# Kernel tuning notes

Hardware: AMD Instinct MI355X
Metric: run time of the kernel (lower is better)

The kernel has to match this reference:

```python
import jax, jax.numpy as jnp
import numpy as np
from jax import lax

B, T, I = 256, 720, 16   # batch, seq_len, input_dim
H = 128                  # hidden_dim
PRED_LEN = 96


def lstm_cell(x, h, c, W_ih, W_hh, b):
    # PyTorch gate order: i, f, g, o ; b = b_ih + b_hh (combined)
    gates = x @ W_ih.T + h @ W_hh.T + b
    i, f, g, o = jnp.split(gates, 4, axis=-1)
    c = jax.nn.sigmoid(f) * c + jax.nn.sigmoid(i) * jnp.tanh(g)
    h = jax.nn.sigmoid(o) * jnp.tanh(c)
    return h, c


def setup_inputs() -> dict:
    key = jax.random.key(0)
    ks = jax.random.split(key, 16)
    k = 1.0 / np.sqrt(H)
    u = lambda kk, shape: jax.random.uniform(kk, shape, jnp.float32, -k, k)
    inp = {
        "x": jax.random.normal(ks[0], (B, T, I), jnp.float32),
        # encoder (bidirectional, 1 layer): forward + backward directions
        "e_Wih_f": u(ks[1], (4 * H, I)), "e_Whh_f": u(ks[2], (4 * H, H)), "e_b_f": u(ks[3], (4 * H,)),
        "e_Wih_b": u(ks[4], (4 * H, I)), "e_Whh_b": u(ks[5], (4 * H, H)), "e_b_b": u(ks[6], (4 * H,)),
        # decoder (bidirectional, 1 layer)
        "d_Wih_f": u(ks[7], (4 * H, I)), "d_Whh_f": u(ks[8], (4 * H, H)), "d_b_f": u(ks[9], (4 * H,)),
        "d_Wih_b": u(ks[10], (4 * H, I)), "d_Whh_b": u(ks[11], (4 * H, H)), "d_b_b": u(ks[12], (4 * H,)),
        # final linear: (2H -> I)
        "W_lin": u(ks[13], (I, 2 * H)), "b_lin": u(ks[14], (I,)),
    }
    return inp


def reference(x, e_Wih_f, e_Whh_f, e_b_f, e_Wih_b, e_Whh_b, e_b_b,
              d_Wih_f, d_Whh_f, d_b_f, d_Wih_b, d_Whh_b, d_b_b,
              W_lin, b_lin):
    xt = jnp.transpose(x, (1, 0, 2))  # [T, B, I] time-major
    h0 = jnp.zeros((B, H), x.dtype)
    c0 = jnp.zeros((B, H), x.dtype)

    # ---- encoder: bidirectional LSTM; only final (h, c) per direction is used ----
    def enc_f(carry, xt_t):
        h, c = lstm_cell(xt_t, carry[0], carry[1], e_Wih_f, e_Whh_f, e_b_f)
        return (h, c), None

    def enc_b(carry, xt_t):
        h, c = lstm_cell(xt_t, carry[0], carry[1], e_Wih_b, e_Whh_b, e_b_b)
        return (h, c), None

    (hf, cf), _ = lax.scan(enc_f, (h0, c0), xt)
    (hb, cb), _ = lax.scan(enc_b, (h0, c0), xt[::-1])

    def dec_step(carry, _):
        inp, hf, cf, hb, cb = carry
        hf, cf = lstm_cell(inp, hf, cf, d_Wih_f, d_Whh_f, d_b_f)
        hb, cb = lstm_cell(inp, hb, cb, d_Wih_b, d_Whh_b, d_b_b)
        # seq_len==1 so out_f = forward hidden, out_b = backward hidden
        out = jnp.concatenate([hf, hb], axis=-1) @ W_lin.T + b_lin  # [B, I]
        return (out, hf, cf, hb, cb), out

    init = (x[:, -1, :], hf, cf, hb, cb)
    _, outs = lax.scan(dec_step, init, None, length=PRED_LEN)  # [P, B, I]
    return jnp.transpose(outs, (1, 0, 2))  # [B, pred_len, I]
```

## Files before the change

kernel.cpp:

```cpp
#include <hip/hip_runtime.h>
#include <math.h>

#define TB    720
#define NI    16
#define NH    128
#define NG    512
#define PRED  96
#define CHUNK 90

typedef _Float16 h2    __attribute__((ext_vector_type(2)));
typedef _Float16 f16x4 __attribute__((ext_vector_type(4)));
typedef _Float16 f16x8 __attribute__((ext_vector_type(8)));
typedef float    f32x4 __attribute__((ext_vector_type(4)));

#define LOG2E  1.4426950408889634f
#define LOG2E2 2.8853900817779268f

__device__ __forceinline__ float rcpf_(float v) {
#if __has_builtin(__builtin_amdgcn_rcpf)
    return __builtin_amdgcn_rcpf(v);
#else
    return 1.0f / v;
#endif
}
__device__ __forceinline__ float ex2(float v) {
#if __has_builtin(__builtin_amdgcn_exp2f)
    return __builtin_amdgcn_exp2f(v);
#else
    return exp2f(v);
#endif
}
__device__ __forceinline__ float sigf(float v)   { return rcpf_(1.0f + __expf(-v)); }
__device__ __forceinline__ float tanhf_(float v) { return 1.0f - 2.0f * rcpf_(1.0f + __expf(2.0f * v)); }

__device__ __forceinline__ unsigned int packf16(float a, float b) {
    h2 p; p.x = (_Float16)a; p.y = (_Float16)b;
    return __builtin_bit_cast(unsigned int, p);
}
__device__ __forceinline__ float2 unpackf16(unsigned int u) {
    h2 p = __builtin_bit_cast(h2, u);
    return make_float2((float)p.x, (float)p.y);
}
__device__ __forceinline__ float fdot2f(unsigned int a, unsigned int b, float c) {
#if __has_builtin(__builtin_amdgcn_fdot2)
    return __builtin_amdgcn_fdot2(__builtin_bit_cast(h2, a), __builtin_bit_cast(h2, b), c, false);
#else
    h2 x = __builtin_bit_cast(h2, a), y = __builtin_bit_cast(h2, b);
    return c + (float)x.x * (float)y.x + (float)x.y * (float)y.y;
#endif
}

__device__ __forceinline__ f16x8 mk8s(const float* p, float s) {
    f16x8 v;
    v[0] = (_Float16)(p[0]  * s); v[1] = (_Float16)(p[1]  * s);
    v[2] = (_Float16)(p[2]  * s); v[3] = (_Float16)(p[3]  * s);
    v[4] = (_Float16)(p[16] * s); v[5] = (_Float16)(p[17] * s);
    v[6] = (_Float16)(p[18] * s); v[7] = (_Float16)(p[19] * s);
    return v;
}
__device__ __forceinline__ f32x4 MFMA(f16x8 a, f16x8 b, f32x4 c) {
    return __builtin_amdgcn_mfma_f32_16x16x32_f16(a, b, c, 0, 0, 0);
}

template <int CTRL, int RMASK>
__device__ __forceinline__ float dppadd(float v) {
    int s = __builtin_bit_cast(int, v);
    int d = __builtin_amdgcn_update_dpp(0, s, CTRL, RMASK, 0xf, true);
    return v + __builtin_bit_cast(float, d);
}

__global__ __launch_bounds__(1024, 4)
void enc_kernel(const float* __restrict__ x,
                const float* __restrict__ Wih_f, const float* __restrict__ Whh_f, const float* __restrict__ b_f,
                const float* __restrict__ Wih_b, const float* __restrict__ Whh_b, const float* __restrict__ b_b,
                float* __restrict__ st)
{
    __shared__ _Float16 hbuf0[16 * NH];
    __shared__ _Float16 hbuf1[16 * NH];
    __shared__ unsigned int xsh[CHUNK * 128];

    const int blk = blockIdx.x;
    const int dir = blk & 1;
    const int b0  = (blk >> 1) << 4;
    const int t   = threadIdx.x;
    const int wv  = t >> 6;
    const int l   = t & 63;
    const int lr  = l & 15;
    const int lk  = l >> 4;

    const float* Wih = dir ? Wih_b : Wih_f;
    const float* Whh = dir ? Whh_b : Whh_f;
    const float* bv  = dir ? b_b   : b_f;

    const int mt0 = 2 * wv, mt1 = 2 * wv + 1;
    const int R0 = mt0 * 16 + lr, R1 = mt1 * 16 + lr;
    const int or0 = (R0 & 3) * 128 + (R0 >> 2);
    const int or1 = (R1 & 3) * 128 + (R1 >> 2);
    const float s0 = ((or0 >> 7) == 2) ? LOG2E2 : LOG2E;
    const float s1 = ((or1 >> 7) == 2) ? LOG2E2 : LOG2E;
    const float* p0 = Whh + (size_t)or0 * NH + lk * 4;
    const float* p1 = Whh + (size_t)or1 * NH + lk * 4;
    f16x8 w0_0 = mk8s(p0, s0), w0_1 = mk8s(p0 + 32, s0), w0_2 = mk8s(p0 + 64, s0), w0_3 = mk8s(p0 + 96, s0);
    f16x8 w1_0 = mk8s(p1, s1), w1_1 = mk8s(p1 + 32, s1), w1_2 = mk8s(p1 + 64, s1), w1_3 = mk8s(p1 + 96, s1);

    f16x8 ax0, ax1;
#define MKAXR(DST, OR, SC) { \
    const float* xr_ = Wih + (size_t)(OR) * NI + lk * 4; \
    DST[0] = (_Float16)(xr_[0] * (SC)); DST[1] = (_Float16)(xr_[1] * (SC)); \
    DST[2] = (_Float16)(xr_[2] * (SC)); DST[3] = (_Float16)(xr_[3] * (SC)); \
    DST[4] = (_Float16)(bv[(OR)] * (SC)); \
    DST[5] = (_Float16)0.f; DST[6] = (_Float16)0.f; DST[7] = (_Float16)0.f; }
    MKAXR(ax0, or0, s0) MKAXR(ax1, or1, s1)
#undef MKAXR

    const int d0 = mt0 * 4 + lk, d1 = mt1 * 4 + lk;

    ((unsigned int*)hbuf0)[t] = 0u;
    float cs0 = 0.f, cs1 = 0.f;

    const int hro0 = 0 * 1024 + lk * 256 + lr * 16;
    const int hro1 = 1 * 1024 + lk * 256 + lr * 16;
    const int hro2 = 2 * 1024 + lk * 256 + lr * 16;
    const int hro3 = 3 * 1024 + lk * 256 + lr * 16;
#define CWB(D) ((((D) >> 5) * 1024) + ((((D) & 15) >> 2) * 256) + lr * 16 + (((((D) & 31) >> 4) * 4 + ((D) & 3)) * 2))
    const int cwb0 = CWB(d0), cwb1 = CWB(d1);
#undef CWB
    const int xoff = lk * 128 + lr * 8;
    const unsigned int oneku = (lk == 0) ? 0x00003c00u : 0u;
    const f32x4 CZ = {0.f, 0.f, 0.f, 0.f};
    __syncthreads();

#define CELL(J, HW) { \
    float ei_ = ex2(-C##J[0]), ef_ = ex2(-C##J[1]); \
    float eg_ = ex2(C##J[2]),  eo_ = ex2(-C##J[3]); \
    float di_ = 1.f + ei_, df_ = 1.f + ef_, dg_ = 1.f + eg_, dq_ = 1.f + eo_; \
    float r1_ = rcpf_(di_ * df_), r2_ = rcpf_(dq_ * dg_); \
    float si_ = r1_ * df_, sf_ = r1_ * di_, so_ = r2_ * dg_; \
    float tg_ = __builtin_fmaf(-2.f * r2_, dq_, 1.f); \
    cs##J = sf_ * cs##J + si_ * tg_; \
    float ec_ = ex2(cs##J * LOG2E2); \
    float th_ = __builtin_fmaf(-2.f, rcpf_(1.f + ec_), 1.f); \
    float hv_ = so_ * th_; \
    *(_Float16*)((char*)(HW) + cwb##J) = (_Float16)hv_; }

#define STEP(HR, HW, SI) { \
    const char* hrb_ = (const char*)(HR); \
    f16x8 bx; \
    { uint2 xq_ = *(const uint2*)((const char*)xsh + (SI) * 512 + xoff); \
      ((unsigned int*)&bx)[0] = xq_.x; ((unsigned int*)&bx)[1] = xq_.y; \
      ((unsigned int*)&bx)[2] = oneku; ((unsigned int*)&bx)[3] = 0u; } \
    f32x4 C0 = MFMA(ax0, bx, CZ); \
    f32x4 C1 = MFMA(ax1, bx, CZ); \
    f16x8 bh_; \
    bh_ = *(const f16x8*)(hrb_ + hro0); \
    C0 = MFMA(w0_0, bh_, C0); C1 = MFMA(w1_0, bh_, C1); \
    bh_ = *(const f16x8*)(hrb_ + hro1); \
    C0 = MFMA(w0_1, bh_, C0); C1 = MFMA(w1_1, bh_, C1); \
    bh_ = *(const f16x8*)(hrb_ + hro2); \
    C0 = MFMA(w0_2, bh_, C0); C1 = MFMA(w1_2, bh_, C1); \
    bh_ = *(const f16x8*)(hrb_ + hro3); \
    C0 = MFMA(w0_3, bh_, C0); C1 = MFMA(w1_3, bh_, C1); \
    CELL(0, HW) CELL(1, HW) \
    __syncthreads(); }

    for (int c = 0; c < 8; ++c) {
        {
            const int c0 = c * CHUNK;
            for (int i = t; i < 16 * CHUNK * 8; i += 1024) {
                const int br  = i / (CHUNK * 8);
                const int rem = i - br * (CHUNK * 8);
                const int ti  = rem >> 3;
                const int dw  = rem & 7;
                const int s_  = c0 + ti;
                const int tt  = dir ? (TB - 1 - s_) : s_;
                float2 v = *(const float2*)(x + ((size_t)(b0 + br) * TB + tt) * NI + dw * 2);
                xsh[ti * 128 + (dw >> 1) * 32 + br * 2 + (dw & 1)] = packf16(v.x, v.y);
            }
        }
        __syncthreads();
        for (int si2 = 0; si2 < CHUNK / 2; ++si2) {
            STEP(hbuf0, hbuf1, si2 * 2)
            STEP(hbuf1, hbuf0, si2 * 2 + 1)
        }
    }
#undef STEP
#undef CELL

    {
        const size_t base = ((size_t)(b0 + lr) * 2 + dir) * 2 * NH;
#define FIN(J) { \
        float hv_ = (float)*(const _Float16*)((const char*)hbuf0 + cwb##J); \
        st[base + d##J] = hv_; st[base + NH + d##J] = cs##J; }
        FIN(0) FIN(1)
#undef FIN
    }
}

#define R8(F)  F(0)F(1)F(2)F(3)F(4)F(5)F(6)F(7)
#define R36_(F) F(8)F(9)F(10)F(11)F(12)F(13)F(14)F(15)F(16)F(17)F(18)F(19)F(20)F(21)F(22)F(23)F(24)F(25)F(26)F(27)F(28)F(29)F(30)F(31)F(32)F(33)F(34)F(35)
#define R36(F) R8(F) R36_(F)
#define R64(F) R36(F) F(36)F(37)F(38)F(39)F(40)F(41)F(42)F(43)F(44)F(45)F(46)F(47)F(48)F(49)F(50)F(51)F(52)F(53)F(54)F(55)F(56)F(57)F(58)F(59)F(60)F(61)F(62)F(63)

#define QD(Q,i0,i1,i2,i3) { a0 = fdot2f((Q).x, w##i0, a0); a1 = fdot2f((Q).y, w##i1, a1); \
                            a2 = fdot2f((Q).z, w##i2, a2); a3 = fdot2f((Q).w, w##i3, a3); }
#define QDU(Q,i0,i1,i2,i3) { a0 = fdot2f((Q).x, u##i0, a0); a1 = fdot2f((Q).y, u##i1, a1); \
                             a2 = fdot2f((Q).z, u##i2, a2); a3 = fdot2f((Q).w, u##i3, a3); }

__global__ __launch_bounds__(1024, 1)
void dec_kernel(const float* __restrict__ x,
                const float* __restrict__ Wih_f, const float* __restrict__ Whh_f, const float* __restrict__ b_f,
                const float* __restrict__ Wih_b, const float* __restrict__ Whh_b, const float* __restrict__ b_b,
                const float* __restrict__ Wlin, const float* __restrict__ blin,
                const float* __restrict__ st, float* __restrict__ out)
{
    __shared__ unsigned int hFh[NH / 2], hBh[NH / 2];
    __shared__ unsigned int inpH[NI / 2];
    __shared__ float g[1024];
    __shared__ float obuf[PRED * 16];

    const int b    = blockIdx.x;
    const int t    = threadIdx.x;
    const int cell = t >> 9;
    const int r    = t & 511;
    const int w    = t >> 6;
    const int ln   = t & 63;

    const float* Wih = cell ? Wih_b : Wih_f;
    const float* Whh = cell ? Whh_b : Whh_f;
    const float* bv  = cell ? b_b   : b_f;

#define DW(K) unsigned int w##K;
    R64(DW)
#undef DW
#define DU(K) unsigned int u##K;
    R8(DU)
#undef DU
    {
        const float* xr = Wih + r * NI;
        const float* hr = Whh + r * NH;
#define LU(K) u##K = packf16(xr[2*(K)], xr[2*(K)+1]);
        R8(LU)
#undef LU
#define LH(K) w##K = packf16(hr[2*(K)], hr[2*(K)+1]);
        R64(LH)
#undef LH
    }
    const float bias = bv[r];

    const float wl0 = Wlin[w * 256 + ln * 4 + 0];
    const float wl1 = Wlin[w * 256 + ln * 4 + 1];
    const float wl2 = Wlin[w * 256 + ln * 4 + 2];
    const float wl3 = Wlin[w * 256 + ln * 4 + 3];
    const float blw = blin[w];

    float cc = 0.0f;
    if (t < 64) {
        const float* sh = st + ((b * 2 + 0) * 2 + 0) * NH;
        hFh[t] = packf16(sh[2 * t], sh[2 * t + 1]);
    } else if (t < 128) {
        const float* sh = st + ((b * 2 + 1) * 2 + 0) * NH;
        hBh[t - 64] = packf16(sh[2 * (t - 64)], sh[2 * (t - 64) + 1]);
    }
    if (t < NH) cc = st[((b * 2 + 0) * 2 + 1) * NH + t];
    else if (t >= 512 && t < 512 + NH) cc = st[((b * 2 + 1) * 2 + 1) * NH + (t - 512)];
    if (t < 8) {
        float2 v = ((const float2*)(x + (size_t)b * TB * NI + (TB - 1) * NI))[t];
        inpH[t] = packf16(v.x, v.y);
    }
    __syncthreads();

    for (int s = 0; s < PRED; ++s) {
        float a0 = bias, a1 = 0.f, a2 = 0.f, a3 = 0.f;
        uint4 q;
        {
            const uint4* xv = (const uint4*)inpH;
            q = xv[0]; QDU(q, 0, 1, 2, 3)
            q = xv[1]; QDU(q, 4, 5, 6, 7)
        }
        const uint4* hv = cell ? (const uint4*)hBh : (const uint4*)hFh;
        q = hv[0];  QD(q, 0, 1, 2, 3)
        q = hv[1];  QD(q, 4, 5, 6, 7)
        q = hv[2];  QD(q, 8, 9, 10, 11)
        q = hv[3];  QD(q, 12, 13, 14, 15)
        q = hv[4];  QD(q, 16, 17, 18, 19)
        q = hv[5];  QD(q, 20, 21, 22, 23)
        q = hv[6];  QD(q, 24, 25, 26, 27)
        q = hv[7];  QD(q, 28, 29, 30, 31)
        q = hv[8];  QD(q, 32, 33, 34, 35)
        q = hv[9];  QD(q, 36, 37, 38, 39)
        q = hv[10]; QD(q, 40, 41, 42, 43)
        q = hv[11]; QD(q, 44, 45, 46, 47)
        q = hv[12]; QD(q, 48, 49, 50, 51)
        q = hv[13]; QD(q, 52, 53, 54, 55)
        q = hv[14]; QD(q, 56, 57, 58, 59)
        q = hv[15]; QD(q, 60, 61, 62, 63)
        g[t] = (a0 + a1) + (a2 + a3);
        __syncthreads();

        if ((t < NH) || (t >= 512 && t < 512 + NH)) {
            float gi = g[t], gf = g[t + NH], gg = g[t + 2 * NH], go = g[t + 3 * NH];
            cc = sigf(gf) * cc + sigf(gi) * tanhf_(gg);
            float h = sigf(go) * tanhf_(cc);
            if (t < NH) ((_Float16*)hFh)[t] = (_Float16)h;
            else        ((_Float16*)hBh)[t - 512] = (_Float16)h;
        }
        __syncthreads();

        {
            const unsigned int* hsrc = (ln < 32) ? (hFh + 2 * ln) : (hBh + 2 * (ln - 32));
            uint2 hw = *(const uint2*)hsrc;
            float2 va = unpackf16(hw.x), vb = unpackf16(hw.y);
            float p = va.x * wl0 + va.y * wl1 + vb.x * wl2 + vb.y * wl3;
            p = dppadd<0x111, 0xf>(p);
            p = dppadd<0x112, 0xf>(p);
            p = dppadd<0x114, 0xf>(p);
            p = dppadd<0x118, 0xf>(p);
            p = dppadd<0x142, 0xa>(p);
            p = dppadd<0x143, 0xc>(p);
            if (ln == 63) {
                float o = p + blw;
                obuf[s * NI + w] = o;
                ((_Float16*)inpH)[w] = (_Float16)o;
            }
        }
        __syncthreads();
    }

    {
        float4* dst = (float4*)(out + (size_t)b * PRED * NI);
        const float4* src = (const float4*)obuf;
        for (int i = t; i < PRED * NI / 4; i += 1024) dst[i] = src[i];
    }
}

extern "C" void kernel_launch(void* const* d_in, const int* in_sizes, int n_in,
                              void* d_out, int out_size, void* d_ws, size_t ws_size,
                              hipStream_t stream)
{
    const float* x      = (const float*)d_in[0];
    const float* eWih_f = (const float*)d_in[1];
    const float* eWhh_f = (const float*)d_in[2];
    const float* eb_f   = (const float*)d_in[3];
    const float* eWih_b = (const float*)d_in[4];
    const float* eWhh_b = (const float*)d_in[5];
    const float* eb_b   = (const float*)d_in[6];
    const float* dWih_f = (const float*)d_in[7];
    const float* dWhh_f = (const float*)d_in[8];
    const float* db_f   = (const float*)d_in[9];
    const float* dWih_b = (const float*)d_in[10];
    const float* dWhh_b = (const float*)d_in[11];
    const float* db_b   = (const float*)d_in[12];
    const float* Wlin   = (const float*)d_in[13];
    const float* blin   = (const float*)d_in[14];

    float* st = (float*)d_ws;

    enc_kernel<<<32, 1024, 0, stream>>>(x, eWih_f, eWhh_f, eb_f, eWih_b, eWhh_b, eb_b, st);
    dec_kernel<<<256, 1024, 0, stream>>>(x, dWih_f, dWhh_f, db_f, dWih_b, dWhh_b, db_b,
                                         Wlin, blin, st, (float*)d_out);
}
```

Measured before the change: 717.1 us.

## Batch decoder over 16 samples per block using MFMA for gates and linear

Replaces the per-sample decoder, which did one block per batch element using packed fp16 dot products, with a batched decoder that handles 16 samples per block. Gate matmuls and the output linear projection run on MFMA instructions, reusing the encoder's layout and fused sigmoid/tanh cell math. This aims to cut per-step latency and sync count in the autoregressive loop. It adds a large shared output buffer and leaves only 16 blocks, so occupancy is low.

```diff
diff --git a/kernel.cpp b/kernel.cpp
--- a/kernel.cpp
+++ b/kernel.cpp
@@ -30,26 +30,14 @@
     return exp2f(v);
 #endif
 }
-__device__ __forceinline__ float sigf(float v)   { return rcpf_(1.0f + __expf(-v)); }
-__device__ __forceinline__ float tanhf_(float v) { return 1.0f - 2.0f * rcpf_(1.0f + __expf(2.0f * v)); }
 
 __device__ __forceinline__ unsigned int packf16(float a, float b) {
     h2 p; p.x = (_Float16)a; p.y = (_Float16)b;
     return __builtin_bit_cast(unsigned int, p);
 }
-__device__ __forceinline__ float2 unpackf16(unsigned int u) {
-    h2 p = __builtin_bit_cast(h2, u);
-    return make_float2((float)p.x, (float)p.y);
-}
-__device__ __forceinline__ float fdot2f(unsigned int a, unsigned int b, float c) {
-#if __has_builtin(__builtin_amdgcn_fdot2)
-    return __builtin_amdgcn_fdot2(__builtin_bit_cast(h2, a), __builtin_bit_cast(h2, b), c, false);
-#else
-    h2 x = __builtin_bit_cast(h2, a), y = __builtin_bit_cast(h2, b);
-    return c + (float)x.x * (float)y.x + (float)x.y * (float)y.y;
-#endif
-}
-
+__device__ __forceinline__ f32x4 MFMA(f16x8 a, f16x8 b, f32x4 c) {
+    return __builtin_amdgcn_mfma_f32_16x16x32_f16(a, b, c, 0, 0, 0);
+}
 __device__ __forceinline__ f16x8 mk8s(const float* p, float s) {
     f16x8 v;
     v[0] = (_Float16)(p[0]  * s); v[1] = (_Float16)(p[1]  * s);
@@ -58,16 +46,20 @@
     v[6] = (_Float16)(p[18] * s); v[7] = (_Float16)(p[19] * s);
     return v;
 }
-__device__ __forceinline__ f32x4 MFMA(f16x8 a, f16x8 b, f32x4 c) {
-    return __builtin_amdgcn_mfma_f32_16x16x32_f16(a, b, c, 0, 0, 0);
-}
-
-template <int CTRL, int RMASK>
-__device__ __forceinline__ float dppadd(float v) {
-    int s = __builtin_bit_cast(int, v);
-    int d = __builtin_amdgcn_update_dpp(0, s, CTRL, RMASK, 0xf, true);
-    return v + __builtin_bit_cast(float, d);
-}
+__device__ __forceinline__ int opaque(int v) { asm volatile("" : "+v"(v)); return v; }
+
+#define CELLBODY(CV, CS, HWPTR, CWBV) { \
+    float ei_ = ex2(-(CV)[0]), ef_ = ex2(-(CV)[1]); \
+    float eg_ = ex2((CV)[2]),  eo_ = ex2(-(CV)[3]); \
+    float di_ = 1.f + ei_, df_ = 1.f + ef_, dg_ = 1.f + eg_, dq_ = 1.f + eo_; \
+    float r1_ = rcpf_(di_ * df_), r2_ = rcpf_(dq_ * dg_); \
+    float si_ = r1_ * df_, sf_ = r1_ * di_, so_ = r2_ * dg_; \
+    float tg_ = __builtin_fmaf(-2.f * r2_, dq_, 1.f); \
+    (CS) = sf_ * (CS) + si_ * tg_; \
+    float ec_ = ex2((CS) * LOG2E2); \
+    float th_ = __builtin_fmaf(-2.f, rcpf_(1.f + ec_), 1.f); \
+    float hv_ = so_ * th_; \
+    *(_Float16*)((char*)(HWPTR) + (CWBV)) = (_Float16)hv_; }
 
 __global__ __launch_bounds__(1024, 4)
 void enc_kernel(const float* __restrict__ x,
@@ -129,19 +121,6 @@
     const unsigned int oneku = (lk == 0) ? 0x00003c00u : 0u;
     const f32x4 CZ = {0.f, 0.f, 0.f, 0.f};
     __syncthreads();
-
-#define CELL(J, HW) { \
-    float ei_ = ex2(-C##J[0]), ef_ = ex2(-C##J[1]); \
-    float eg_ = ex2(C##J[2]),  eo_ = ex2(-C##J[3]); \
-    float di_ = 1.f + ei_, df_ = 1.f + ef_, dg_ = 1.f + eg_, dq_ = 1.f + eo_; \
-    float r1_ = rcpf_(di_ * df_), r2_ = rcpf_(dq_ * dg_); \
-    float si_ = r1_ * df_, sf_ = r1_ * di_, so_ = r2_ * dg_; \
-    float tg_ = __builtin_fmaf(-2.f * r2_, dq_, 1.f); \
-    cs##J = sf_ * cs##J + si_ * tg_; \
-    float ec_ = ex2(cs##J * LOG2E2); \
-    float th_ = __builtin_fmaf(-2.f, rcpf_(1.f + ec_), 1.f); \
-    float hv_ = so_ * th_; \
-    *(_Float16*)((char*)(HW) + cwb##J) = (_Float16)hv_; }
 
 #define STEP(HR, HW, SI) { \
     const char* hrb_ = (const char*)(HR); \
@@ -160,7 +139,8 @@
     C0 = MFMA(w0_2, bh_, C0); C1 = MFMA(w1_2, bh_, C1); \
     bh_ = *(const f16x8*)(hrb_ + hro3); \
     C0 = MFMA(w0_3, bh_, C0); C1 = MFMA(w1_3, bh_, C1); \
-    CELL(0, HW) CELL(1, HW) \
+    CELLBODY(C0, cs0, HW, cwb0) \
+    CELLBODY(C1, cs1, HW, cwb1) \
     __syncthreads(); }
 
     for (int c = 0; c < 8; ++c) {
@@ -184,152 +164,170 @@
         }
     }
 #undef STEP
-#undef CELL
 
     {
         const size_t base = ((size_t)(b0 + lr) * 2 + dir) * 2 * NH;
-#define FIN(J) { \
-        float hv_ = (float)*(const _Float16*)((const char*)hbuf0 + cwb##J); \
-        st[base + d##J] = hv_; st[base + NH + d##J] = cs##J; }
-        FIN(0) FIN(1)
-#undef FIN
-    }
-}
-
-#define R8(F)  F(0)F(1)F(2)F(3)F(4)F(5)F(6)F(7)
-#define R36_(F) F(8)F(9)F(10)F(11)F(12)F(13)F(14)F(15)F(16)F(17)F(18)F(19)F(20)F(21)F(22)F(23)F(24)F(25)F(26)F(27)F(28)F(29)F(30)F(31)F(32)F(33)F(34)F(35)
-#define R36(F) R8(F) R36_(F)
-#define R64(F) R36(F) F(36)F(37)F(38)F(39)F(40)F(41)F(42)F(43)F(44)F(45)F(46)F(47)F(48)F(49)F(50)F(51)F(52)F(53)F(54)F(55)F(56)F(57)F(58)F(59)F(60)F(61)F(62)F(63)
-
-#define QD(Q,i0,i1,i2,i3) { a0 = fdot2f((Q).x, w##i0, a0); a1 = fdot2f((Q).y, w##i1, a1); \
-                            a2 = fdot2f((Q).z, w##i2, a2); a3 = fdot2f((Q).w, w##i3, a3); }
-#define QDU(Q,i0,i1,i2,i3) { a0 = fdot2f((Q).x, u##i0, a0); a1 = fdot2f((Q).y, u##i1, a1); \
-                             a2 = fdot2f((Q).z, u##i2, a2); a3 = fdot2f((Q).w, u##i3, a3); }
-
-__global__ __launch_bounds__(1024, 1)
+#define CWB(D) ((((D) >> 5) * 1024) + ((((D) & 15) >> 2) * 256) + lr * 16 + (((((D) & 31) >> 4) * 4 + ((D) & 3)) * 2))
+        st[base + d0]      = (float)*(const _Float16*)((const char*)hbuf0 + CWB(d0));
+        st[base + NH + d0] = cs0;
+        st[base + d1]      = (float)*(const _Float16*)((const char*)hbuf0 + CWB(d1));
+        st[base + NH + d1] = cs1;
+#undef CWB
+    }
+}
+
+__global__ __launch_bounds__(1024, 4)
 void dec_kernel(const float* __restrict__ x,
                 const float* __restrict__ Wih_f, const float* __restrict__ Whh_f, const float* __restrict__ b_f,
                 const float* __restrict__ Wih_b, const float* __restrict__ Whh_b, const float* __restrict__ b_b,
                 const float* __restrict__ Wlin, const float* __restrict__ blin,
                 const float* __restrict__ st, float* __restrict__ out)
 {
-    __shared__ unsigned int hFh[NH / 2], hBh[NH / 2];
-    __shared__ unsigned int inpH[NI / 2];
-    __shared__ float g[1024];
-    __shared__ float obuf[PRED * 16];
-
-    const int b    = blockIdx.x;
+    __shared__ _Float16 hF0[16 * NH], hF1[16 * NH];
+    __shared__ _Float16 hB0[16 * NH], hB1[16 * NH];
+    __shared__ unsigned int wlin_s[8 * 64 * 4];
+    __shared__ unsigned int inpH[16 * 8];
+    __shared__ float obuf[PRED * 16 * 16];
+
+    const int b0   = blockIdx.x << 4;
     const int t    = threadIdx.x;
-    const int cell = t >> 9;
-    const int r    = t & 511;
-    const int w    = t >> 6;
-    const int ln   = t & 63;
+    const int wv   = t >> 6;
+    const int cell = wv >> 3;
+    const int wvv  = wv & 7;
+    const int l    = t & 63;
+    const int lr   = l & 15;
+    const int lk   = l >> 4;
 
     const float* Wih = cell ? Wih_b : Wih_f;
     const float* Whh = cell ? Whh_b : Whh_f;
     const float* bv  = cell ? b_b   : b_f;
 
-#define DW(K) unsigned int w##K;
-    R64(DW)
-#undef DW
-#define DU(K) unsigned int u##K;
-    R8(DU)
-#undef DU
+    if (t < 512) {
+        const int f = t >> 6, ll = t & 63;
+        const int elr = ll & 15, elk = ll >> 4;
+        const float* wr = Wlin + elr * 256 + f * 32 + elk * 4;
+        uint4 q;
+        q.x = packf16(wr[0],  wr[1]);  q.y = packf16(wr[2],  wr[3]);
+        q.z = packf16(wr[16], wr[17]); q.w = packf16(wr[18], wr[19]);
+        *(uint4*)&wlin_s[(f * 64 + ll) * 4] = q;
+    }
+
+    const int mt0 = 4 * wvv, mt1 = 4 * wvv + 1, mt2 = 4 * wvv + 2, mt3 = 4 * wvv + 3;
+    const int R0 = mt0 * 16 + lr, R1 = mt1 * 16 + lr, R2 = mt2 * 16 + lr, R3 = mt3 * 16 + lr;
+    const int or0 = (R0 & 3) * 128 + (R0 >> 2);
+    const int or1 = (R1 & 3) * 128 + (R1 >> 2);
+    const int or2 = (R2 & 3) * 128 + (R2 >> 2);
+    const int or3 = (R3 & 3) * 128 + (R3 >> 2);
+    const float s0 = ((or0 >> 7) == 2) ? LOG2E2 : LOG2E;
+    const float s1 = ((or1 >> 7) == 2) ? LOG2E2 : LOG2E;
+    const float s2 = ((or2 >> 7) == 2) ? LOG2E2 : LOG2E;
+    const float s3 = ((or3 >> 7) == 2) ? LOG2E2 : LOG2E;
+    const float* p0 = Whh + (size_t)or0 * NH + lk * 4;
+    const float* p1 = Whh + (size_t)or1 * NH + lk * 4;
+    const float* p2 = Whh + (size_t)or2 * NH + lk * 4;
+    const float* p3 = Whh + (size_t)or3 * NH + lk * 4;
+    f16x8 w0_0 = mk8s(p0, s0), w0_1 = mk8s(p0 + 32, s0), w0_2 = mk8s(p0 + 64, s0), w0_3 = mk8s(p0 + 96, s0);
+    f16x8 w1_0 = mk8s(p1, s1), w1_1 = mk8s(p1 + 32, s1), w1_2 = mk8s(p1 + 64, s1), w1_3 = mk8s(p1 + 96, s1);
+    f16x8 w2_0 = mk8s(p2, s2), w2_1 = mk8s(p2 + 32, s2), w2_2 = mk8s(p2 + 64, s2), w2_3 = mk8s(p2 + 96, s2);
+    f16x8 w3_0 = mk8s(p3, s3), w3_1 = mk8s(p3 + 32, s3), w3_2 = mk8s(p3 + 64, s3), w3_3 = mk8s(p3 + 96, s3);
+
+    f16x8 ax0, ax1, ax2, ax3;
+#define MKAXR(DST, OR, SC) { \
+    const float* xr_ = Wih + (size_t)(OR) * NI + lk * 4; \
+    DST[0] = (_Float16)(xr_[0] * (SC)); DST[1] = (_Float16)(xr_[1] * (SC)); \
+    DST[2] = (_Float16)(xr_[2] * (SC)); DST[3] = (_Float16)(xr_[3] * (SC)); \
+    DST[4] = (_Float16)(bv[(OR)] * (SC)); \
+    DST[5] = (_Float16)0.f; DST[6] = (_Float16)0.f; DST[7] = (_Float16)0.f; }
+    MKAXR(ax0, or0, s0) MKAXR(ax1, or1, s1) MKAXR(ax2, or2, s2) MKAXR(ax3, or3, s3)
+#undef MKAXR
+
+    const int d0 = mt0 * 4 + lk, d1 = mt1 * 4 + lk, d2 = mt2 * 4 + lk, d3 = mt3 * 4 + lk;
+
+    const int hro0 = 0 * 1024 + lk * 256 + lr * 16;
+    const int hro1 = 1 * 1024 + lk * 256 + lr * 16;
+    const int hro2 = 2 * 1024 + lk * 256 + lr * 16;
+    const int hro3 = 3 * 1024 + lk * 256 + lr * 16;
+#define CWB(D) ((((D) >> 5) * 1024) + ((((D) & 15) >> 2) * 256) + lr * 16 + (((((D) & 31) >> 4) * 4 + ((D) & 3)) * 2))
+    const int cwb0 = CWB(d0), cwb1 = CWB(d1), cwb2 = CWB(d2), cwb3 = CWB(d3);
+    float cs0, cs1, cs2, cs3;
     {
-        const float* xr = Wih + r * NI;
-        const float* hr = Whh + r * NH;
-#define LU(K) u##K = packf16(xr[2*(K)], xr[2*(K)+1]);
-        R8(LU)
-#undef LU
-#define LH(K) w##K = packf16(hr[2*(K)], hr[2*(K)+1]);
-        R64(LH)
-#undef LH
-    }
-    const float bias = bv[r];
-
-    const float wl0 = Wlin[w * 256 + ln * 4 + 0];
-    const float wl1 = Wlin[w * 256 + ln * 4 + 1];
-    const float wl2 = Wlin[w * 256 + ln * 4 + 2];
-    const float wl3 = Wlin[w * 256 + ln * 4 + 3];
-    const float blw = blin[w];
-
-    float cc = 0.0f;
-    if (t < 64) {
-        const float* sh = st + ((b * 2 + 0) * 2 + 0) * NH;
-        hFh[t] = packf16(sh[2 * t], sh[2 * t + 1]);
-    } else if (t < 128) {
-        const float* sh = st + ((b * 2 + 1) * 2 + 0) * NH;
-        hBh[t - 64] = packf16(sh[2 * (t - 64)], sh[2 * (t - 64) + 1]);
-    }
-    if (t < NH) cc = st[((b * 2 + 0) * 2 + 1) * NH + t];
-    else if (t >= 512 && t < 512 + NH) cc = st[((b * 2 + 1) * 2 + 1) * NH + (t - 512)];
-    if (t < 8) {
-        float2 v = ((const float2*)(x + (size_t)b * TB * NI + (TB - 1) * NI))[t];
-        inpH[t] = packf16(v.x, v.y);
-    }
+        _Float16* hini = cell ? hB0 : hF0;
+        const size_t bs = ((size_t)(b0 + lr) * 2 + cell) * 2 * NH;
+        *(_Float16*)((char*)hini + cwb0) = (_Float16)st[bs + d0];  cs0 = st[bs + NH + d0];
+        *(_Float16*)((char*)hini + cwb1) = (_Float16)st[bs + d1];  cs1 = st[bs + NH + d1];
+        *(_Float16*)((char*)hini + cwb2) = (_Float16)st[bs + d2];  cs2 = st[bs + NH + d2];
+        *(_Float16*)((char*)hini + cwb3) = (_Float16)st[bs + d3];  cs3 = st[bs + NH + d3];
+    }
+#undef CWB
+    if (t < 128) {
+        const int ilr = t >> 3, idw = t & 7;
+        const float2 v = *(const float2*)(x + ((size_t)(b0 + ilr) * TB + (TB - 1)) * NI + idw * 2);
+        inpH[ilr * 8 + idw] = packf16(v.x, v.y);
+    }
+    const float bl0 = blin[4 * lk + 0], bl1 = blin[4 * lk + 1];
+    const float bl2 = blin[4 * lk + 2], bl3 = blin[4 * lk + 3];
+    const unsigned int oneku = (lk == 0) ? 0x00003c00u : 0u;
+    const f32x4 CZ = {0.f, 0.f, 0.f, 0.f};
     __syncthreads();
 
-    for (int s = 0; s < PRED; ++s) {
-        float a0 = bias, a1 = 0.f, a2 = 0.f, a3 = 0.f;
-        uint4 q;
-        {
-            const uint4* xv = (const uint4*)inpH;
-            q = xv[0]; QDU(q, 0, 1, 2, 3)
-            q = xv[1]; QDU(q, 4, 5, 6, 7)
-        }
-        const uint4* hv = cell ? (const uint4*)hBh : (const uint4*)hFh;
-        q = hv[0];  QD(q, 0, 1, 2, 3)
-        q = hv[1];  QD(q, 4, 5, 6, 7)
-        q = hv[2];  QD(q, 8, 9, 10, 11)
-        q = hv[3];  QD(q, 12, 13, 14, 15)
-        q = hv[4];  QD(q, 16, 17, 18, 19)
-        q = hv[5];  QD(q, 20, 21, 22, 23)
-        q = hv[6];  QD(q, 24, 25, 26, 27)
-        q = hv[7];  QD(q, 28, 29, 30, 31)
-        q = hv[8];  QD(q, 32, 33, 34, 35)
-        q = hv[9];  QD(q, 36, 37, 38, 39)
-        q = hv[10]; QD(q, 40, 41, 42, 43)
-        q = hv[11]; QD(q, 44, 45, 46, 47)
-        q = hv[12]; QD(q, 48, 49, 50, 51)
-        q = hv[13]; QD(q, 52, 53, 54, 55)
-        q = hv[14]; QD(q, 56, 57, 58, 59)
-        q = hv[15]; QD(q, 60, 61, 62, 63)
-        g[t] = (a0 + a1) + (a2 + a3);
-        __syncthreads();
-
-        if ((t < NH) || (t >= 512 && t < 512 + NH)) {
-            float gi = g[t], gf = g[t + NH], gg = g[t + 2 * NH], go = g[t + 3 * NH];
-            cc = sigf(gf) * cc + sigf(gi) * tanhf_(gg);
-            float h = sigf(go) * tanhf_(cc);
-            if (t < NH) ((_Float16*)hFh)[t] = (_Float16)h;
-            else        ((_Float16*)hBh)[t - 512] = (_Float16)h;
-        }
-        __syncthreads();
-
-        {
-            const unsigned int* hsrc = (ln < 32) ? (hFh + 2 * ln) : (hBh + 2 * (ln - 32));
-            uint2 hw = *(const uint2*)hsrc;
-            float2 va = unpackf16(hw.x), vb = unpackf16(hw.y);
-            float p = va.x * wl0 + va.y * wl1 + vb.x * wl2 + vb.y * wl3;
-            p = dppadd<0x111, 0xf>(p);
-            p = dppadd<0x112, 0xf>(p);
-            p = dppadd<0x114, 0xf>(p);
-            p = dppadd<0x118, 0xf>(p);
-            p = dppadd<0x142, 0xa>(p);
-            p = dppadd<0x143, 0xc>(p);
-            if (ln == 63) {
-                float o = p + blw;
-                obuf[s * NI + w] = o;
-                ((_Float16*)inpH)[w] = (_Float16)o;
-            }
-        }
-        __syncthreads();
-    }
-
-    {
-        float4* dst = (float4*)(out + (size_t)b * PRED * NI);
-        const float4* src = (const float4*)obuf;
-        for (int i = t; i < PRED * NI / 4; i += 1024) dst[i] = src[i];
+#define STEPD(HRF, HWF, HRB, HWB, S) { \
+    const char* hr_ = cell ? (const char*)(HRB) : (const char*)(HRF); \
+    char*       hw_ = cell ? (char*)(HWB)       : (char*)(HWF); \
+    f16x8 bx; \
+    { uint2 xq_ = *(const uint2*)((const char*)inpH + lr * 32 + lk * 8); \
+      ((unsigned int*)&bx)[0] = xq_.x; ((unsigned int*)&bx)[1] = xq_.y; \
+      ((unsigned int*)&bx)[2] = oneku; ((unsigned int*)&bx)[3] = 0u; } \
+    f32x4 C0 = MFMA(ax0, bx, CZ); f32x4 C1 = MFMA(ax1, bx, CZ); \
+    f32x4 C2 = MFMA(ax2, bx, CZ); f32x4 C3 = MFMA(ax3, bx, CZ); \
+    f16x8 bh_; \
+    bh_ = *(const f16x8*)(hr_ + hro0); \
+    C0 = MFMA(w0_0, bh_, C0); C1 = MFMA(w1_0, bh_, C1); \
+    C2 = MFMA(w2_0, bh_, C2); C3 = MFMA(w3_0, bh_, C3); \
+    bh_ = *(const f16x8*)(hr_ + hro1); \
+    C0 = MFMA(w0_1, bh_, C0); C1 = MFMA(w1_1, bh_, C1); \
+    C2 = MFMA(w2_1, bh_, C2); C3 = MFMA(w3_1, bh_, C3); \
+    bh_ = *(const f16x8*)(hr_ + hro2); \
+    C0 = MFMA(w0_2, bh_, C0); C1 = MFMA(w1_2, bh_, C1); \
+    C2 = MFMA(w2_2, bh_, C2); C3 = MFMA(w3_2, bh_, C3); \
+    bh_ = *(const f16x8*)(hr_ + hro3); \
+    C0 = MFMA(w0_3, bh_, C0); C1 = MFMA(w1_3, bh_, C1); \
+    C2 = MFMA(w2_3, bh_, C2); C3 = MFMA(w3_3, bh_, C3); \
+    CELLBODY(C0, cs0, hw_, cwb0) \
+    CELLBODY(C1, cs1, hw_, cwb1) \
+    CELLBODY(C2, cs2, hw_, cwb2) \
+    CELLBODY(C3, cs3, hw_, cwb3) \
+    __syncthreads(); \
+    if (wv == 0) { \
+        f32x4 P = CZ; \
+        f16x8 af_, bf_; \
+        _Pragma("unroll") \
+        for (int f = 0; f < 8; ++f) { \
+            af_ = *(const f16x8*)((const char*)wlin_s + opaque((f * 64 + l) * 16)); \
+            const char* hb_ = (f < 4) ? (const char*)(HWF) + f * 1024 \
+                                      : (const char*)(HWB) + (f - 4) * 1024; \
+            bf_ = *(const f16x8*)(hb_ + lk * 256 + lr * 16); \
+            P = MFMA(af_, bf_, P); \
+        } \
+        float o0 = P[0] + bl0, o1 = P[1] + bl1, o2 = P[2] + bl2, o3 = P[3] + bl3; \
+        float* ob_ = obuf + (S) * 256 + (4 * lk) * 16 + lr; \
+        ob_[0] = o0; ob_[16] = o1; ob_[32] = o2; ob_[48] = o3; \
+        inpH[lr * 8 + lk * 2]     = packf16(o0, o1); \
+        inpH[lr * 8 + lk * 2 + 1] = packf16(o2, o3); \
+    } \
+    __syncthreads(); }
+
+    for (int s2 = 0; s2 < PRED / 2; ++s2) {
+        STEPD(hF0, hF1, hB0, hB1, s2 * 2)
+        STEPD(hF1, hF0, hB1, hB0, s2 * 2 + 1)
+    }
+#undef STEPD
+
+    for (int i = t; i < PRED * 256; i += 1024) {
+        const int lr2 = i / (PRED * NI);
+        const int rem = i - lr2 * (PRED * NI);
+        const int s   = rem >> 4;
+        const int j   = rem & 15;
+        out[(size_t)(b0 + lr2) * PRED * NI + rem] = obuf[s * 256 + j * 16 + lr2];
     }
 }
 
@@ -356,6 +354,6 @@
     float* st = (float*)d_ws;
 
     enc_kernel<<<32, 1024, 0, stream>>>(x, eWih_f, eWhh_f, eb_f, eWih_b, eWhh_b, eb_b, st);
-    dec_kernel<<<256, 1024, 0, stream>>>(x, dWih_f, dWhh_f, db_f, dWih_b, dWhh_b, db_b,
-                                         Wlin, blin, st, (float*)d_out);
-}
+    dec_kernel<<<16, 1024, 0, stream>>>(x, dWih_f, dWhh_f, db_f, dWih_b, dWhh_b, db_b,
+                                        Wlin, blin, st, (float*)d_out);
+}
```

After: 734.6 us. 1.02x slower.
